# Kernel optimization log

Measured on AMD Instinct MI355X. Metric: run time of the kernel, lower is better.

Reference implementation:

```python
import jax, jax.numpy as jnp
import numpy as np

NUM_PATCHES = 128  # static stand-in for max(patch_ids)+1


def setup_inputs() -> dict:
    key = jax.random.key(0)
    k1, k2, k3, k4 = jax.random.split(key, 4)
    B, S, H, D = 8, 8192, 512, 768
    byte_hiddens = jax.random.normal(k1, (B, S, H), dtype=jnp.float32)
    patch_ids = jnp.sort(jax.random.randint(k2, (B, S), 0, NUM_PATCHES), axis=-1)
    # Dense output_projection (glorot-uniform-ish init)
    lim = float(np.sqrt(6.0 / (H + D)))
    W_proj = jax.random.uniform(k3, (H, D), minval=-lim, maxval=lim, dtype=jnp.float32)
    b_proj = jnp.zeros((D,), dtype=jnp.float32)
    return {"byte_hiddens": byte_hiddens, "W_proj": W_proj, "b_proj": b_proj,
            "patch_ids": patch_ids}


def reference(byte_hiddens, W_proj, b_proj, patch_ids):
    # Mean pooling within patches: for each patch p, mean of byte_hiddens where
    # patch_ids == p (sum / max(count, 1)), then Dense projection.
    B, S, H = byte_hiddens.shape
    P = NUM_PATCHES
    # Flatten batch into segment ids so one segment_sum covers all (b, p) pairs.
    seg = (patch_ids + jnp.arange(B, dtype=patch_ids.dtype)[:, None] * P).reshape(-1)
    flat = byte_hiddens.reshape(B * S, H)
    sums = jax.ops.segment_sum(flat, seg, num_segments=B * P)          # [B*P, H]
    counts = jax.ops.segment_sum(jnp.ones((B * S,), byte_hiddens.dtype), seg,
                                 num_segments=B * P)                   # [B*P]
    means = sums / jnp.maximum(counts, 1.0)[:, None]                   # [B*P, H]
    means = means.reshape(B, P, H)
    return means @ W_proj + b_proj                                     # [B, P, D]
```

## Files before the change

### kernel.cpp

```cpp
#include <hip/hip_runtime.h>

#define B_ 8
#define S_ 8192
#define H_ 512
#define D_ 768
#define P_ 128

typedef __attribute__((ext_vector_type(8))) short bf16x8;
typedef __attribute__((ext_vector_type(4))) float f32x4;

static __device__ inline unsigned short f2bf(float f) {
    unsigned int u = __float_as_uint(f);
    unsigned int r = (u + 0x7fffu + ((u >> 16) & 1u)) >> 16;
    return (unsigned short)r;
}


__global__ __launch_bounds__(256) void pool_wt_kernel(
    const float* __restrict__ bh, const int* __restrict__ ids,
    const float* __restrict__ W,
    unsigned short* __restrict__ means, unsigned short* __restrict__ Wt)
{
    __shared__ __align__(16) char smem[64 * 72 * sizeof(unsigned short)];
    const int bid = blockIdx.x;
    const int t = threadIdx.x;

    if (bid < P_ * B_) {
        const int p = bid & (P_ - 1);
        const int b = bid >> 7;
        const int c = t & 127;
        const int r_ofs = t >> 7;

        const int* row = ids + (size_t)b * S_;
        int lo0 = 0, hi0 = S_, lo1 = 0, hi1 = S_;
        #pragma unroll
        for (int it = 0; it < 13; ++it) {
            int m0 = (lo0 + hi0) >> 1, m1 = (lo1 + hi1) >> 1;
            int v0 = row[m0], v1 = row[m1];
            if (v0 < p)  lo0 = m0 + 1; else hi0 = m0;
            if (v1 <= p) lo1 = m1 + 1; else hi1 = m1;
        }
        const int start = lo0;
        const int cnt   = lo1 - lo0;

        const float4* src = (const float4*)(bh + ((size_t)b * S_ + (size_t)start) * H_) + c;
        float4 a0 = {0.f, 0.f, 0.f, 0.f};
        float4 a1 = {0.f, 0.f, 0.f, 0.f};
        int r = r_ofs;
        for (; r + 2 < cnt; r += 4) {
            float4 v0 = src[(size_t)r * (H_ / 4)];
            float4 v1 = src[(size_t)(r + 2) * (H_ / 4)];
            a0.x += v0.x; a0.y += v0.y; a0.z += v0.z; a0.w += v0.w;
            a1.x += v1.x; a1.y += v1.y; a1.z += v1.z; a1.w += v1.w;
        }
        if (r < cnt) {
            float4 v = src[(size_t)r * (H_ / 4)];
            a0.x += v.x; a0.y += v.y; a0.z += v.z; a0.w += v.w;
        }
        float4 s;
        s.x = a0.x + a1.x; s.y = a0.y + a1.y; s.z = a0.z + a1.z; s.w = a0.w + a1.w;

        float4* red = (float4*)smem;
        if (r_ofs == 1) red[c] = s;
        __syncthreads();
        if (r_ofs == 0) {
            float4 o = red[c];
            const float inv = 1.0f / (float)(cnt > 0 ? cnt : 1);
            ushort4 w;
            w.x = f2bf((s.x + o.x) * inv);
            w.y = f2bf((s.y + o.y) * inv);
            w.z = f2bf((s.z + o.z) * inv);
            w.w = f2bf((s.w + o.w) * inv);
            *(ushort4*)&means[((size_t)(b * P_ + p)) * H_ + c * 4] = w;
        }
    } else {
        const int id = bid - P_ * B_;
        const int nb = (id % (D_ / 64)) * 64;
        const int kb = (id / (D_ / 64)) * 64;
        unsigned short (*T)[72] = (unsigned short (*)[72])smem;
        {
            const int kk = t >> 4;
            const int nn = (t & 15) * 4;
            #pragma unroll
            for (int i = 0; i < 4; ++i) {
                float4 v = *(const float4*)&W[(size_t)(kb + kk + i * 16) * D_ + nb + nn];
                T[nn + 0][kk + i * 16] = f2bf(v.x);
                T[nn + 1][kk + i * 16] = f2bf(v.y);
                T[nn + 2][kk + i * 16] = f2bf(v.z);
                T[nn + 3][kk + i * 16] = f2bf(v.w);
            }
        }
        __syncthreads();
        {
            const int nn = t >> 4;
            const int kk = (t & 15) * 4;
            #pragma unroll
            for (int i = 0; i < 4; ++i) {
                ushort4 o;
                o.x = T[nn + i * 16][kk + 0];
                o.y = T[nn + i * 16][kk + 1];
                o.z = T[nn + i * 16][kk + 2];
                o.w = T[nn + i * 16][kk + 3];
                *(ushort4*)&Wt[(size_t)(nb + nn + i * 16) * H_ + kb + kk] = o;
            }
        }
    }
}

__global__ __launch_bounds__(256) void gemm_kernel(
    const unsigned short* __restrict__ A, const unsigned short* __restrict__ Bt,
    const float* __restrict__ bias, float* __restrict__ C)
{
    __shared__ unsigned short As[64][72];
    __shared__ unsigned short Bs[64][72];

    const int t    = threadIdx.x;
    const int lane = t & 63;
    const int wv   = t >> 6;
    const int mrow = lane & 15;
    const int quad = lane >> 4;
    const int m0   = blockIdx.y * 64;
    const int n0   = blockIdx.x * 64;

    const int sr = t >> 2;
    const int sk = (t & 3) * 16;
    const unsigned short* Aptr = A  + (size_t)(m0 + sr) * H_ + sk;
    const unsigned short* Bptr = Bt + (size_t)(n0 + sr) * H_ + sk;

    uint4 a0 = *(const uint4*)Aptr;
    uint4 a1 = *(const uint4*)(Aptr + 8);
    uint4 b0 = *(const uint4*)Bptr;
    uint4 b1 = *(const uint4*)(Bptr + 8);

    f32x4 acc[4] = {};

    for (int k0 = 0; k0 < H_; k0 += 64) {
        *(uint4*)&As[sr][sk]     = a0;
        *(uint4*)&As[sr][sk + 8] = a1;
        *(uint4*)&Bs[sr][sk]     = b0;
        *(uint4*)&Bs[sr][sk + 8] = b1;
        __syncthreads();

        if (k0 + 64 < H_) {
            a0 = *(const uint4*)(Aptr + k0 + 64);
            a1 = *(const uint4*)(Aptr + k0 + 72);
            b0 = *(const uint4*)(Bptr + k0 + 64);
            b1 = *(const uint4*)(Bptr + k0 + 72);
        }

        #pragma unroll
        for (int kk = 0; kk < 2; ++kk) {
            bf16x8 af = *(const bf16x8*)&As[wv * 16 + mrow][kk * 32 + quad * 8];
            #pragma unroll
            for (int t4 = 0; t4 < 4; ++t4) {
                bf16x8 bf = *(const bf16x8*)&Bs[t4 * 16 + mrow][kk * 32 + quad * 8];
                acc[t4] = __builtin_amdgcn_mfma_f32_16x16x32_bf16(af, bf, acc[t4], 0, 0, 0);
            }
        }
        __syncthreads();
    }

    #pragma unroll
    for (int t4 = 0; t4 < 4; ++t4) {
        const int col = n0 + t4 * 16 + mrow;
        const float bia = bias[col];
        #pragma unroll
        for (int r = 0; r < 4; ++r) {
            const int rowi = m0 + wv * 16 + quad * 4 + r;
            C[(size_t)rowi * D_ + col] = acc[t4][r] + bia;
        }
    }
}

extern "C" void kernel_launch(void* const* d_in, const int* in_sizes, int n_in,
                              void* d_out, int out_size, void* d_ws, size_t ws_size,
                              hipStream_t stream) {
    const float* bh   = (const float*)d_in[0];
    const float* W    = (const float*)d_in[1];
    const float* bias = (const float*)d_in[2];
    const int*   ids  = (const int*)d_in[3];
    float* out = (float*)d_out;

    unsigned short* means = (unsigned short*)d_ws;
    unsigned short* Wt    = means + (size_t)B_ * P_ * H_;

    pool_wt_kernel<<<dim3(P_ * B_ + (D_ / 64) * (H_ / 64)), 256, 0, stream>>>(
        bh, ids, W, means, Wt);
    gemm_kernel<<<dim3(D_ / 64, (B_ * P_) / 64), 256, 0, stream>>>(
        means, Wt, bias, out);
}
```

Baseline: 207.2 us.

## Speed up patch search with ballot coarse search, deepen pooling unroll, widen GEMM K-tile

```diff
diff --git a/kernel.cpp b/kernel.cpp
--- a/kernel.cpp
+++ b/kernel.cpp
@@ -32,10 +32,25 @@
         const int r_ofs = t >> 7;
 
         const int* row = ids + (size_t)b * S_;
-        int lo0 = 0, hi0 = S_, lo1 = 0, hi1 = S_;
-        #pragma unroll
-        for (int it = 0; it < 13; ++it) {
-            int m0 = (lo0 + hi0) >> 1, m1 = (lo1 + hi1) >> 1;
+
+        const int v = row[t * 32];
+        const unsigned long long bal0 = __ballot(v < p);
+        const unsigned long long bal1 = __ballot(v <= p);
+        int* cnts = (int*)(smem + 2048);
+        if ((t & 63) == 0) {
+            cnts[t >> 6]       = __popcll(bal0);
+            cnts[4 + (t >> 6)] = __popcll(bal1);
+        }
+        __syncthreads();
+        const int c0 = cnts[0] + cnts[1] + cnts[2] + cnts[3];
+        const int c1 = cnts[4] + cnts[5] + cnts[6] + cnts[7];
+
+        int lo0 = c0 ? 32 * (c0 - 1) + 1 : 0, hi0 = 32 * c0;
+        int lo1 = c1 ? 32 * (c1 - 1) + 1 : 0, hi1 = 32 * c1;
+        #pragma unroll
+        for (int it = 0; it < 5; ++it) {
+            int m0 = (lo0 + hi0) >> 1; if (m0 > S_ - 1) m0 = S_ - 1;
+            int m1 = (lo1 + hi1) >> 1; if (m1 > S_ - 1) m1 = S_ - 1;
             int v0 = row[m0], v1 = row[m1];
             if (v0 < p)  lo0 = m0 + 1; else hi0 = m0;
             if (v1 <= p) lo1 = m1 + 1; else hi1 = m1;
@@ -46,19 +61,28 @@
         const float4* src = (const float4*)(bh + ((size_t)b * S_ + (size_t)start) * H_) + c;
         float4 a0 = {0.f, 0.f, 0.f, 0.f};
         float4 a1 = {0.f, 0.f, 0.f, 0.f};
+        float4 a2 = {0.f, 0.f, 0.f, 0.f};
+        float4 a3 = {0.f, 0.f, 0.f, 0.f};
         int r = r_ofs;
-        for (; r + 2 < cnt; r += 4) {
+        for (; r + 6 < cnt; r += 8) {
             float4 v0 = src[(size_t)r * (H_ / 4)];
             float4 v1 = src[(size_t)(r + 2) * (H_ / 4)];
+            float4 v2 = src[(size_t)(r + 4) * (H_ / 4)];
+            float4 v3 = src[(size_t)(r + 6) * (H_ / 4)];
             a0.x += v0.x; a0.y += v0.y; a0.z += v0.z; a0.w += v0.w;
             a1.x += v1.x; a1.y += v1.y; a1.z += v1.z; a1.w += v1.w;
-        }
-        if (r < cnt) {
-            float4 v = src[(size_t)r * (H_ / 4)];
-            a0.x += v.x; a0.y += v.y; a0.z += v.z; a0.w += v.w;
+            a2.x += v2.x; a2.y += v2.y; a2.z += v2.z; a2.w += v2.w;
+            a3.x += v3.x; a3.y += v3.y; a3.z += v3.z; a3.w += v3.w;
+        }
+        for (; r < cnt; r += 2) {
+            float4 v0 = src[(size_t)r * (H_ / 4)];
+            a0.x += v0.x; a0.y += v0.y; a0.z += v0.z; a0.w += v0.w;
         }
         float4 s;
-        s.x = a0.x + a1.x; s.y = a0.y + a1.y; s.z = a0.z + a1.z; s.w = a0.w + a1.w;
+        s.x = (a0.x + a1.x) + (a2.x + a3.x);
+        s.y = (a0.y + a1.y) + (a2.y + a3.y);
+        s.z = (a0.z + a1.z) + (a2.z + a3.z);
+        s.w = (a0.w + a1.w) + (a2.w + a3.w);
 
         float4* red = (float4*)smem;
         if (r_ofs == 1) red[c] = s;
@@ -111,8 +135,8 @@
     const unsigned short* __restrict__ A, const unsigned short* __restrict__ Bt,
     const float* __restrict__ bias, float* __restrict__ C)
 {
-    __shared__ unsigned short As[64][72];
-    __shared__ unsigned short Bs[64][72];
+    __shared__ unsigned short As[64][136];
+    __shared__ unsigned short Bs[64][136];
 
     const int t    = threadIdx.x;
     const int lane = t & 63;
@@ -123,33 +147,37 @@
     const int n0   = blockIdx.x * 64;
 
     const int sr = t >> 2;
-    const int sk = (t & 3) * 16;
+    const int sk = (t & 3) * 32;
     const unsigned short* Aptr = A  + (size_t)(m0 + sr) * H_ + sk;
     const unsigned short* Bptr = Bt + (size_t)(n0 + sr) * H_ + sk;
 
-    uint4 a0 = *(const uint4*)Aptr;
-    uint4 a1 = *(const uint4*)(Aptr + 8);
-    uint4 b0 = *(const uint4*)Bptr;
-    uint4 b1 = *(const uint4*)(Bptr + 8);
+    uint4 a[4], b[4];
+    #pragma unroll
+    for (int i = 0; i < 4; ++i) {
+        a[i] = *(const uint4*)(Aptr + i * 8);
+        b[i] = *(const uint4*)(Bptr + i * 8);
+    }
 
     f32x4 acc[4] = {};
 
-    for (int k0 = 0; k0 < H_; k0 += 64) {
-        *(uint4*)&As[sr][sk]     = a0;
-        *(uint4*)&As[sr][sk + 8] = a1;
-        *(uint4*)&Bs[sr][sk]     = b0;
-        *(uint4*)&Bs[sr][sk + 8] = b1;
-        __syncthreads();
-
-        if (k0 + 64 < H_) {
-            a0 = *(const uint4*)(Aptr + k0 + 64);
-            a1 = *(const uint4*)(Aptr + k0 + 72);
-            b0 = *(const uint4*)(Bptr + k0 + 64);
-            b1 = *(const uint4*)(Bptr + k0 + 72);
-        }
-
-        #pragma unroll
-        for (int kk = 0; kk < 2; ++kk) {
+    for (int k0 = 0; k0 < H_; k0 += 128) {
+        #pragma unroll
+        for (int i = 0; i < 4; ++i) {
+            *(uint4*)&As[sr][sk + i * 8] = a[i];
+            *(uint4*)&Bs[sr][sk + i * 8] = b[i];
+        }
+        __syncthreads();
+
+        if (k0 + 128 < H_) {
+            #pragma unroll
+            for (int i = 0; i < 4; ++i) {
+                a[i] = *(const uint4*)(Aptr + k0 + 128 + i * 8);
+                b[i] = *(const uint4*)(Bptr + k0 + 128 + i * 8);
+            }
+        }
+
+        #pragma unroll
+        for (int kk = 0; kk < 4; ++kk) {
             bf16x8 af = *(const bf16x8*)&As[wv * 16 + mrow][kk * 32 + quad * 8];
             #pragma unroll
             for (int t4 = 0; t4 < 4; ++t4) {
```

After: 214.2 us. +3.4%, slower.

## Narrow patch search with ballot sampling and double-buffer GEMM LDS tiles

Applied to the files above, without the earlier changes.

```diff
diff --git a/kernel.cpp b/kernel.cpp
--- a/kernel.cpp
+++ b/kernel.cpp
@@ -32,10 +32,25 @@
         const int r_ofs = t >> 7;
 
         const int* row = ids + (size_t)b * S_;
-        int lo0 = 0, hi0 = S_, lo1 = 0, hi1 = S_;
+
+        const int v = row[t * 32];
+        const unsigned long long bal0 = __ballot(v < p);
+        const unsigned long long bal1 = __ballot(v <= p);
+        int* cnts = (int*)(smem + 2048);
+        if ((t & 63) == 0) {
+            cnts[t >> 6]       = __popcll(bal0);
+            cnts[4 + (t >> 6)] = __popcll(bal1);
+        }
+        __syncthreads();
+        const int c0 = cnts[0] + cnts[1] + cnts[2] + cnts[3];
+        const int c1 = cnts[4] + cnts[5] + cnts[6] + cnts[7];
+
+        int lo0 = c0 ? 32 * (c0 - 1) + 1 : 0, hi0 = 32 * c0;
+        int lo1 = c1 ? 32 * (c1 - 1) + 1 : 0, hi1 = 32 * c1;
         #pragma unroll
-        for (int it = 0; it < 13; ++it) {
-            int m0 = (lo0 + hi0) >> 1, m1 = (lo1 + hi1) >> 1;
+        for (int it = 0; it < 5; ++it) {
+            int m0 = (lo0 + hi0) >> 1; if (m0 > S_ - 1) m0 = S_ - 1;
+            int m1 = (lo1 + hi1) >> 1; if (m1 > S_ - 1) m1 = S_ - 1;
             int v0 = row[m0], v1 = row[m1];
             if (v0 < p)  lo0 = m0 + 1; else hi0 = m0;
             if (v1 <= p) lo1 = m1 + 1; else hi1 = m1;
@@ -54,8 +69,8 @@
             a1.x += v1.x; a1.y += v1.y; a1.z += v1.z; a1.w += v1.w;
         }
         if (r < cnt) {
-            float4 v = src[(size_t)r * (H_ / 4)];
-            a0.x += v.x; a0.y += v.y; a0.z += v.z; a0.w += v.w;
+            float4 v2 = src[(size_t)r * (H_ / 4)];
+            a0.x += v2.x; a0.y += v2.y; a0.z += v2.z; a0.w += v2.w;
         }
         float4 s;
         s.x = a0.x + a1.x; s.y = a0.y + a1.y; s.z = a0.z + a1.z; s.w = a0.w + a1.w;
@@ -111,8 +126,8 @@
     const unsigned short* __restrict__ A, const unsigned short* __restrict__ Bt,
     const float* __restrict__ bias, float* __restrict__ C)
 {
-    __shared__ unsigned short As[64][72];
-    __shared__ unsigned short Bs[64][72];
+    __shared__ unsigned short As[2][64][72];
+    __shared__ unsigned short Bs[2][64][72];
 
     const int t    = threadIdx.x;
     const int lane = t & 63;
@@ -132,16 +147,18 @@
     uint4 b0 = *(const uint4*)Bptr;
     uint4 b1 = *(const uint4*)(Bptr + 8);
 
+    *(uint4*)&As[0][sr][sk]     = a0;
+    *(uint4*)&As[0][sr][sk + 8] = a1;
+    *(uint4*)&Bs[0][sr][sk]     = b0;
+    *(uint4*)&Bs[0][sr][sk + 8] = b1;
+
     f32x4 acc[4] = {};
+    int cur = 0;
+    __syncthreads();
 
     for (int k0 = 0; k0 < H_; k0 += 64) {
-        *(uint4*)&As[sr][sk]     = a0;
-        *(uint4*)&As[sr][sk + 8] = a1;
-        *(uint4*)&Bs[sr][sk]     = b0;
-        *(uint4*)&Bs[sr][sk + 8] = b1;
-        __syncthreads();
-
-        if (k0 + 64 < H_) {
+        const bool more = (k0 + 64 < H_);
+        if (more) {
             a0 = *(const uint4*)(Aptr + k0 + 64);
             a1 = *(const uint4*)(Aptr + k0 + 72);
             b0 = *(const uint4*)(Bptr + k0 + 64);
@@ -150,14 +167,22 @@
 
         #pragma unroll
         for (int kk = 0; kk < 2; ++kk) {
-            bf16x8 af = *(const bf16x8*)&As[wv * 16 + mrow][kk * 32 + quad * 8];
+            bf16x8 af = *(const bf16x8*)&As[cur][wv * 16 + mrow][kk * 32 + quad * 8];
             #pragma unroll
             for (int t4 = 0; t4 < 4; ++t4) {
-                bf16x8 bf = *(const bf16x8*)&Bs[t4 * 16 + mrow][kk * 32 + quad * 8];
+                bf16x8 bf = *(const bf16x8*)&Bs[cur][t4 * 16 + mrow][kk * 32 + quad * 8];
                 acc[t4] = __builtin_amdgcn_mfma_f32_16x16x32_bf16(af, bf, acc[t4], 0, 0, 0);
             }
         }
-        __syncthreads();
+
+        if (more) {
+            *(uint4*)&As[cur ^ 1][sr][sk]     = a0;
+            *(uint4*)&As[cur ^ 1][sr][sk + 8] = a1;
+            *(uint4*)&Bs[cur ^ 1][sr][sk]     = b0;
+            *(uint4*)&Bs[cur ^ 1][sr][sk + 8] = b1;
+            __syncthreads();
+        }
+        cur ^= 1;
     }
 
     #pragma unroll
```

Result: no change. 206.0 us (-0.6%).
